# Performance work log

Measured on AMD Instinct MI355X. Metric: run time of the kernel, lower is better.

Reference implementation:

```python
import jax, jax.numpy as jnp
import numpy as np
from jax.scipy import special

B, N, DIM, H, DK, DV, F = 2, 1536, 1536, 8, 64, 64, 192


def _pos_embed(seq_len, feat):
    """Enformer relative positional basis: [2*seq_len-1, feat]."""
    per = feat // 6  # 3 basis families x (symmetric, antisymmetric)
    d = jnp.arange(-seq_len + 1, seq_len, dtype=jnp.float32)
    ad = jnp.abs(d)[:, None]  # [2N-1, 1]
    # exponential decay, log-spaced half lives
    half_life = 2.0 ** jnp.linspace(3.0, float(np.log2(seq_len)), per)
    expo = jnp.exp(-jnp.log(2.0) / half_life * ad)
    # central binary mask
    widths = 2.0 ** jnp.arange(1, per + 1, dtype=jnp.float32) - 1.0
    cmask = (widths > ad).astype(jnp.float32)
    # gamma pdf basis
    stddev = seq_len / (2.0 * per)
    start_mean = seq_len / per
    mean = jnp.linspace(start_mean, float(seq_len), per)
    conc = (mean / stddev) ** 2
    rate = mean / stddev ** 2
    log_unnorm = special.xlogy(conc - 1.0, ad) - rate * ad
    log_norm = special.gammaln(conc) - conc * jnp.log(rate)
    probs = jnp.exp(log_unnorm - log_norm) + 1e-8
    gamma = probs / jnp.max(probs, axis=-1, keepdims=True)
    emb = jnp.concatenate([expo, cmask, gamma], axis=-1)
    emb = jnp.concatenate([emb, jnp.sign(d)[:, None] * emb], axis=-1)
    return emb.astype(jnp.float32)


def _relative_shift(x):
    # x: [B, H, N, 2N-1] -> [B, H, N, N] (Transformer-XL shift)
    b, h, t1, t2 = x.shape
    x = jnp.pad(x, ((0, 0), (0, 0), (0, 0), (1, 0)))  # [B,H,N,2N]
    x = x.reshape(b, h, t2 + 1, t1)[:, :, 1:, :].reshape(b, h, t1, t2)
    return x[..., : (t2 + 2) // 2]


def setup_inputs() -> dict:
    key = jax.random.key(0)
    ks = jax.random.split(key, 8)
    s = 0.02
    return {
        "x": jax.random.normal(ks[0], (B, N, DIM), dtype=jnp.float32),
        "Wq": jax.random.normal(ks[1], (DIM, H * DK), dtype=jnp.float32) * s,
        "Wk": jax.random.normal(ks[2], (DIM, H * DK), dtype=jnp.float32) * s,
        "Wv": jax.random.normal(ks[3], (DIM, H * DV), dtype=jnp.float32) * s,
        "Wrel": jax.random.normal(ks[4], (F, H * DK), dtype=jnp.float32) * s,
        "Wout": jax.random.normal(ks[5], (H * DV, DIM), dtype=jnp.float32) * s,
        "bout": jnp.zeros((DIM,), dtype=jnp.float32),
        "rel_content_bias": jax.random.normal(ks[6], (1, H, 1, DK), dtype=jnp.float32),
        "rel_pos_bias": jax.random.normal(ks[7], (1, H, 1, DK), dtype=jnp.float32),
        "pos_embed": _pos_embed(N, F),  # [2N-1, F] buffer
    }


def reference(x, Wq, Wk, Wv, Wrel, Wout, bout, rel_content_bias, rel_pos_bias, pos_embed):
    b, n, _ = x.shape
    h, dk = rel_content_bias.shape[1], rel_content_bias.shape[3]
    dv = Wv.shape[1] // h
    scale = dk ** -0.5
    q = (x @ Wq).reshape(b, n, h, dk).transpose(0, 2, 1, 3) * scale  # [b,h,n,dk]
    k = (x @ Wk).reshape(b, n, h, dk).transpose(0, 2, 1, 3)
    v = (x @ Wv).reshape(b, n, h, dv).transpose(0, 2, 1, 3)
    content_logits = jnp.einsum('bhid,bhjd->bhij', q + rel_content_bias, k)
    rel_k = (pos_embed @ Wrel).reshape(-1, h, dk).transpose(1, 0, 2)  # [h,2n-1,dk]
    rel_logits = jnp.einsum('bhid,hjd->bhij', q + rel_pos_bias, rel_k)  # [b,h,n,2n-1]
    rel_logits = _relative_shift(rel_logits)  # [b,h,n,n]
    attn = jax.nn.softmax(content_logits + rel_logits, axis=-1)
    out = jnp.einsum('bhij,bhjd->bhid', attn, v)
    out = out.transpose(0, 2, 1, 3).reshape(b, n, h * dv)
    return out @ Wout + bout
```

## Files before the change

### kernel.cpp

```cpp
#include <hip/hip_runtime.h>

#define NSEQ  1536
#define HEADS 8
#define NREL  3071
#define NRELP 3072

typedef __bf16 bf16;
typedef __bf16 bf16x8 __attribute__((ext_vector_type(8)));
typedef __bf16 bf16x4 __attribute__((ext_vector_type(4)));
typedef float  f32x4  __attribute__((ext_vector_type(4)));

static __device__ __forceinline__ f32x4 mfma16(bf16x8 a, bf16x8 b, f32x4 c) {
  return __builtin_amdgcn_mfma_f32_16x16x32_bf16(a, b, c, 0, 0, 0);
}

static __device__ __forceinline__ void gload_lds16(const bf16* g, bf16* l) {
  __builtin_amdgcn_global_load_lds((const __attribute__((address_space(1))) void*)g,
                                   (__attribute__((address_space(3))) void*)l, 16, 0, 0);
}

#define DPP_F(v, ctrl) __int_as_float(__builtin_amdgcn_update_dpp(0, __float_as_int(v), ctrl, 0xF, 0xF, true))
static __device__ __forceinline__ float rowsum16(float v) {
  v += DPP_F(v, 0xB1);
  v += DPP_F(v, 0x4E);
  v += DPP_F(v, 0x124);
  v += DPP_F(v, 0x128);
  return v;
}

__global__ __launch_bounds__(256) void prep(const float* __restrict__ x, const float* __restrict__ pos,
                                            const float* __restrict__ Wq, const float* __restrict__ Wk,
                                            const float* __restrict__ Wv, const float* __restrict__ Wout,
                                            const float* __restrict__ Wrel,
                                            bf16* __restrict__ xb, bf16* __restrict__ posb,
                                            bf16* __restrict__ WT, bf16* __restrict__ WoT,
                                            bf16* __restrict__ WrT) {
  int blk = blockIdx.x;
  if (blk < 4608) {
    int i = blk * 256 + threadIdx.x;
    float4 v = ((const float4*)x)[i];
    bf16x4 o;
    o[0] = (bf16)v.x; o[1] = (bf16)v.y; o[2] = (bf16)v.z; o[3] = (bf16)v.w;
    ((bf16x4*)xb)[i] = o;
    return;
  }
  blk -= 4608;
  if (blk < 576) {
    int i = blk * 256 + threadIdx.x;
    if (i < (NREL * 192 / 4)) {
      float4 v = ((const float4*)pos)[i];
      bf16x4 o;
      o[0] = (bf16)v.x; o[1] = (bf16)v.y; o[2] = (bf16)v.z; o[3] = (bf16)v.w;
      ((bf16x4*)posb)[i] = o;
    }
    return;
  }
  blk -= 576;
  const float* in; bf16* out; int C, ostride, orowoff, cx, ry;
  if (blk < 768)       { in = Wq;   out = WT;  C = 512;  ostride = 1536; orowoff = 0;    cx = blk % 16; ry = blk / 16; }
  else if (blk < 1536) { blk -= 768;  in = Wk;   out = WT;  C = 512;  ostride = 1536; orowoff = 512;  cx = blk % 16; ry = blk / 16; }
  else if (blk < 2304) { blk -= 1536; in = Wv;   out = WT;  C = 512;  ostride = 1536; orowoff = 1024; cx = blk % 16; ry = blk / 16; }
  else if (blk < 3072) { blk -= 2304; in = Wout; out = WoT; C = 1536; ostride = 512;  orowoff = 0;    cx = blk % 48; ry = blk / 48; }
  else                 { blk -= 3072; in = Wrel; out = WrT; C = 512;  ostride = 192;  orowoff = 0;    cx = blk % 16; ry = blk / 16; }
  __shared__ float t[32][33];
  int tx = threadIdx.x & 31, ty = threadIdx.x >> 5;
  int r0 = ry * 32, c0 = cx * 32;
#pragma unroll
  for (int i = 0; i < 4; i++)
    t[ty + 8 * i][tx] = in[(size_t)(r0 + ty + 8 * i) * C + c0 + tx];
  __syncthreads();
#pragma unroll
  for (int i = 0; i < 4; i++)
    out[(size_t)(c0 + ty + 8 * i + orowoff) * ostride + r0 + tx] = (bf16)t[tx][ty + 8 * i];
}

static __device__ __forceinline__ void gemm_core(const bf16* __restrict__ A, const bf16* __restrict__ BT,
                                                 int Klen, int ldk, int m0, int n0, int M,
                                                 bf16* sa, bf16* sb, f32x4 acc[4][2]) {
  int tid = threadIdx.x, wave = tid >> 6, lane = tid & 63;
  int l15 = lane & 15, quad = lane >> 4;
  int lrow = lane >> 3, lcg = lane & 7;
  for (int k0 = 0; k0 < Klen; k0 += 64) {
    __syncthreads();
#pragma unroll
    for (int t = 0; t < 2; t++) {
      int row = wave * 16 + t * 8 + lrow;
      int ra = m0 + row; if (ra > M - 1) ra = M - 1;
      gload_lds16(A + (size_t)ra * ldk + k0 + ((lcg ^ (row & 7)) * 8), sa + (wave * 16 + t * 8) * 64);
    }
#pragma unroll
    for (int t = 0; t < 4; t++) {
      int row = wave * 32 + t * 8 + lrow;
      gload_lds16(BT + (size_t)(n0 + row) * ldk + k0 + ((lcg ^ (row & 7)) * 8), sb + (wave * 32 + t * 8) * 64);
    }
    __syncthreads();
#pragma unroll
    for (int kq = 0; kq < 2; kq++) {
      bf16x8 af[4], bfr[2];
#pragma unroll
      for (int rt = 0; rt < 4; rt++) {
        int row = rt * 16 + l15;
        af[rt] = *(const bf16x8*)&sa[row * 64 + (((kq * 4 + quad) ^ (row & 7)) * 8)];
      }
#pragma unroll
      for (int ct = 0; ct < 2; ct++) {
        int row = wave * 32 + ct * 16 + l15;
        bfr[ct] = *(const bf16x8*)&sb[row * 64 + (((kq * 4 + quad) ^ (row & 7)) * 8)];
      }
#pragma unroll
      for (int ct = 0; ct < 2; ct++)
#pragma unroll
        for (int rt = 0; rt < 4; rt++)
          acc[rt][ct] = mfma16(af[rt], bfr[ct], acc[rt][ct]);
    }
  }
}

__global__ __launch_bounds__(256) void gemm_qkv(const bf16* __restrict__ xb, const bf16* __restrict__ WT,
                                                const float* __restrict__ cb, const float* __restrict__ pb,
                                                bf16* __restrict__ qc, bf16* __restrict__ qp,
                                                bf16* __restrict__ kb, bf16* __restrict__ vt) {
  __shared__ __align__(16) bf16 sa[64 * 64];
  __shared__ __align__(16) bf16 sb[128 * 64];
  __shared__ __align__(16) bf16 tv[64 * 130];
  int tid = threadIdx.x, wave = tid >> 6, lane = tid & 63;
  int l15 = lane & 15, quad = lane >> 4;
  int m0 = blockIdx.x * 64, n0 = blockIdx.y * 128;
  f32x4 acc[4][2] = {};
  gemm_core(xb, WT, 1536, 1536, m0, n0, 3072, sa, sb, acc);
  int b = m0 / NSEQ, nseq0 = m0 % NSEQ;
  if (blockIdx.y < 8) {
    bool isq = blockIdx.y < 4;
#pragma unroll
    for (int rt = 0; rt < 4; rt++)
#pragma unroll
      for (int ct = 0; ct < 2; ct++)
#pragma unroll
        for (int r = 0; r < 4; r++) {
          int row = nseq0 + rt * 16 + quad * 4 + r;
          int colg = n0 + wave * 32 + ct * 16 + l15;
          int col = colg & 511;
          int h = col >> 6, d = col & 63;
          size_t o = ((size_t)(b * 8 + h) * NSEQ + row) * 64 + d;
          float v = acc[rt][ct][r];
          if (isq) {
            float qv = v * 0.125f;
            qc[o] = (bf16)(qv + cb[col]);
            qp[o] = (bf16)(qv + pb[col]);
          } else {
            kb[o] = (bf16)v;
          }
        }
  } else {
#pragma unroll
    for (int rt = 0; rt < 4; rt++)
#pragma unroll
      for (int ct = 0; ct < 2; ct++)
#pragma unroll
        for (int r = 0; r < 4; r++)
          tv[(rt * 16 + quad * 4 + r) * 130 + wave * 32 + ct * 16 + l15] = (bf16)acc[rt][ct][r];
    __syncthreads();
    int n = tid & 63, c0v = tid >> 6;
    int hbase = (blockIdx.y - 8) * 2;
#pragma unroll
    for (int hh = 0; hh < 2; hh++)
#pragma unroll
      for (int i = 0; i < 16; i++) {
        int dv = i * 4 + c0v;
        vt[((size_t)(b * 8 + hbase + hh) * 64 + dv) * NSEQ + nseq0 + n] = tv[n * 130 + hh * 64 + dv];
      }
  }
}

__global__ __launch_bounds__(256) void gemm_rel(const bf16* __restrict__ posb, const bf16* __restrict__ WrT,
                                                bf16* __restrict__ rk) {
  __shared__ __align__(16) bf16 sa[64 * 64];
  __shared__ __align__(16) bf16 sb[128 * 64];
  int tid = threadIdx.x, wave = tid >> 6, lane = tid & 63;
  int l15 = lane & 15, quad = lane >> 4;
  int m0 = blockIdx.x * 64, n0 = blockIdx.y * 128;
  f32x4 acc[4][2] = {};
  gemm_core(posb, WrT, 192, 192, m0, n0, NREL, sa, sb, acc);
#pragma unroll
  for (int rt = 0; rt < 4; rt++)
#pragma unroll
    for (int ct = 0; ct < 2; ct++)
#pragma unroll
      for (int r = 0; r < 4; r++) {
        int row = m0 + rt * 16 + quad * 4 + r;
        if (row < NREL) {
          int col = n0 + wave * 32 + ct * 16 + l15;
          rk[((size_t)(col >> 6) * NRELP + row) * 64 + (col & 63)] = (bf16)acc[rt][ct][r];
        }
      }
}

__global__ __launch_bounds__(256) void gemm_out(const bf16* __restrict__ A, const bf16* __restrict__ BT,
                                                float* __restrict__ C, const float* __restrict__ bias) {
  __shared__ __align__(16) bf16 sa[64 * 64];
  __shared__ __align__(16) bf16 sb[128 * 64];
  int tid = threadIdx.x, wave = tid >> 6, lane = tid & 63;
  int l15 = lane & 15, quad = lane >> 4;
  int m0 = blockIdx.x * 64, n0 = blockIdx.y * 128;
  f32x4 acc[4][2] = {};
  gemm_core(A, BT, 512, 512, m0, n0, 3072, sa, sb, acc);
#pragma unroll
  for (int rt = 0; rt < 4; rt++)
#pragma unroll
    for (int ct = 0; ct < 2; ct++)
#pragma unroll
      for (int r = 0; r < 4; r++) {
        int row = m0 + rt * 16 + quad * 4 + r;
        int col = n0 + wave * 32 + ct * 16 + l15;
        C[(size_t)row * 1536 + col] = acc[rt][ct][r] + bias[col];
      }
}

__global__ __launch_bounds__(256, 4) void attn(const bf16* __restrict__ qc, const bf16* __restrict__ qp,
                                               const bf16* __restrict__ kb, const bf16* __restrict__ vt,
                                               const bf16* __restrict__ rk,
                                               float* __restrict__ Opart, float* __restrict__ mlp) {
  __shared__ __align__(16) bf16 sk[64 * 64];
  __shared__ __align__(16) bf16 sv[64 * 64];
  __shared__ __align__(16) bf16 srel[128 * 64];
  __shared__ __align__(16) bf16 pls[4][16 * 72];
  int qb = blockIdx.x, bh = blockIdx.y, kz = blockIdx.z;
  int h = bh & 7;
  int i0 = qb * 64;
  int wave = threadIdx.x >> 6, lane = threadIdx.x & 63;
  int l15 = lane & 15, quad = lane >> 4;
  int lrow = lane >> 3, lcg = lane & 7;
  const bf16* qcb = qc + (size_t)bh * NSEQ * 64;
  const bf16* qpb = qp + (size_t)bh * NSEQ * 64;
  const bf16* kbb = kb + (size_t)bh * NSEQ * 64;
  const bf16* vtb = vt + (size_t)bh * 64 * NSEQ;
  const bf16* rkh = rk + (size_t)h * NRELP * 64;
  bf16* plsw = pls[wave];

  int qrow = i0 + wave * 16 + l15;
  bf16x8 aqc0 = *(const bf16x8*)(qcb + (size_t)qrow * 64 + quad * 8);
  bf16x8 aqc1 = *(const bf16x8*)(qcb + (size_t)qrow * 64 + 32 + quad * 8);
  bf16x8 aqp0 = *(const bf16x8*)(qpb + (size_t)qrow * 64 + quad * 8);
  bf16x8 aqp1 = *(const bf16x8*)(qpb + (size_t)qrow * 64 + 32 + quad * 8);

  int bidx[4];
  bool hisel[4];
#pragma unroll
  for (int r = 0; r < 4; r++) {
    int rl = quad * 4 + r;
    bidx[r] = (quad * 16 + ((l15 + 15 - rl) & 15)) << 2;
    hisel[r] = l15 > rl;
  }

  f32x4 acco[4] = {};
  float li[4] = {0.0f, 0.0f, 0.0f, 0.0f};

  int locbase = (3 - wave) * 16;
  for (int jt = 0; jt < 12; jt++) {
    int j0 = kz * 768 + jt * 64;
    int Rbase = 1472 + j0 - i0;
    __syncthreads();
#pragma unroll
    for (int t = 0; t < 2; t++) {
      int row = wave * 16 + t * 8 + lrow;
      gload_lds16(kbb + (size_t)(j0 + row) * 64 + ((lcg ^ (row & 7)) * 8),
                  sk + (wave * 16 + t * 8) * 64);
    }
#pragma unroll
    for (int t = 0; t < 2; t++) {
      int row = wave * 16 + t * 8 + lrow;
      gload_lds16(vtb + (size_t)row * NSEQ + j0 + ((lcg ^ (row & 7)) * 8),
                  sv + (wave * 16 + t * 8) * 64);
    }
#pragma unroll
    for (int t = 0; t < 4; t++) {
      int loc = wave * 32 + t * 8 + lrow;
      gload_lds16(rkh + (size_t)(Rbase + loc) * 64 + ((lcg ^ (loc & 7)) * 8),
                  srel + (wave * 32 + t * 8) * 64);
    }
    __syncthreads();
    f32x4 s[4] = {};
#pragma unroll
    for (int c = 0; c < 4; c++) {
      int key = c * 16 + l15;
      bf16x8 b0 = *(const bf16x8*)&sk[key * 64 + ((quad ^ (key & 7)) * 8)];
      bf16x8 b1 = *(const bf16x8*)&sk[key * 64 + (((4 + quad) ^ (key & 7)) * 8)];
      s[c] = mfma16(aqc0, b0, s[c]);
      s[c] = mfma16(aqc1, b1, s[c]);
    }
    f32x4 sb5[5];
#pragma unroll
    for (int cc = 0; cc < 5; cc++) {
      int loc = locbase + cc * 16 + l15;
      bf16x8 b0 = *(const bf16x8*)&srel[loc * 64 + ((quad ^ (loc & 7)) * 8)];
      bf16x8 b1 = *(const bf16x8*)&srel[loc * 64 + (((4 + quad) ^ (loc & 7)) * 8)];
      f32x4 z = {};
      z = mfma16(aqp0, b0, z);
      sb5[cc] = mfma16(aqp1, b1, z);
    }
#pragma unroll
    for (int r = 0; r < 4; r++) {
      float bp[5];
#pragma unroll
      for (int cc = 0; cc < 5; cc++)
        bp[cc] = __int_as_float(__builtin_amdgcn_ds_bpermute(bidx[r], __float_as_int(sb5[cc][r])));
#pragma unroll
      for (int c = 0; c < 4; c++)
        s[c][r] += hisel[r] ? bp[c + 1] : bp[c];
    }
#pragma unroll
    for (int c = 0; c < 4; c++)
#pragma unroll
      for (int r = 0; r < 4; r++) {
        float p = __expf(s[c][r] - 8.0f);
        bf16 pbh = (bf16)p;
        li[r] += (float)pbh;
        plsw[(quad * 4 + r) * 72 + c * 16 + l15] = pbh;
      }
#pragma unroll
    for (int ks = 0; ks < 2; ks++) {
      bf16x8 ap = *(const bf16x8*)&plsw[l15 * 72 + ks * 32 + quad * 8];
#pragma unroll
      for (int c = 0; c < 4; c++) {
        int dv = c * 16 + l15;
        bf16x8 bv = *(const bf16x8*)&sv[dv * 64 + (((ks * 4 + quad) ^ (dv & 7)) * 8)];
        acco[c] = mfma16(ap, bv, acco[c]);
      }
    }
  }
#pragma unroll
  for (int r = 0; r < 4; r++)
    li[r] = rowsum16(li[r]);
  int qt16 = qb * 4 + wave;
  size_t pbase = ((size_t)(bh * 96 + qt16) * 2 + kz);
#pragma unroll
  for (int c = 0; c < 4; c++)
#pragma unroll
    for (int r = 0; r < 4; r++)
      Opart[pbase * 1024 + (quad * 4 + r) * 64 + c * 16 + l15] = acco[c][r];
  if (l15 == 0) {
#pragma unroll
    for (int r = 0; r < 4; r++)
      mlp[pbase * 16 + quad * 4 + r] = li[r];
  }
}

__global__ void attn_merge(const float* __restrict__ Opart, const float* __restrict__ mlp,
                           bf16* __restrict__ O) {
  int qt = blockIdx.x, bh = blockIdx.y;
  int b = bh >> 3, h = bh & 7;
  int col = threadIdx.x & 63, rg = threadIdx.x >> 6;
  size_t base = (size_t)(bh * 96 + qt) * 2;
#pragma unroll
  for (int rr = 0; rr < 4; rr++) {
    int row = rg * 4 + rr;
    float L = mlp[base * 16 + row] + mlp[(base + 1) * 16 + row];
    float v = Opart[base * 1024 + row * 64 + col] + Opart[(base + 1) * 1024 + row * 64 + col];
    O[((size_t)(b * NSEQ + qt * 16 + row) * 8 + h) * 64 + col] = (bf16)(v / L);
  }
}

extern "C" void kernel_launch(void* const* d_in, const int* in_sizes, int n_in,
                              void* d_out, int out_size, void* d_ws, size_t ws_size,
                              hipStream_t stream) {
  const float* x    = (const float*)d_in[0];
  const float* Wq   = (const float*)d_in[1];
  const float* Wk   = (const float*)d_in[2];
  const float* Wv   = (const float*)d_in[3];
  const float* Wrel = (const float*)d_in[4];
  const float* Wout = (const float*)d_in[5];
  const float* bout = (const float*)d_in[6];
  const float* cb   = (const float*)d_in[7];
  const float* pb   = (const float*)d_in[8];
  const float* pos  = (const float*)d_in[9];
  float* out = (float*)d_out;

  char* ws = (char*)d_ws;
  size_t off = 0;
  auto alloc = [&](size_t bytes) {
    char* p = ws + off;
    off = (off + bytes + 255) & ~(size_t)255;
    return p;
  };
  bf16*  xb    = (bf16*)alloc(3072UL * 1536 * 2);
  bf16*  WT    = (bf16*)alloc(1536UL * 1536 * 2);
  bf16*  WoT   = (bf16*)alloc(1536UL * 512 * 2);
  bf16*  WrT   = (bf16*)alloc(512UL * 192 * 2);
  bf16*  posb  = (bf16*)alloc((size_t)NREL * 192 * 2);
  bf16*  qcb   = (bf16*)alloc(16UL * NSEQ * 64 * 2);
  bf16*  qpb   = (bf16*)alloc(16UL * NSEQ * 64 * 2);
  bf16*  kbb   = (bf16*)alloc(16UL * NSEQ * 64 * 2);
  bf16*  vtb   = (bf16*)alloc(16UL * NSEQ * 64 * 2);
  bf16*  rkb   = (bf16*)alloc(8UL * NRELP * 64 * 2);
  bf16*  Ob    = (bf16*)alloc(3072UL * 512 * 2);
  float* Opart = (float*)alloc(16UL * 96 * 2 * 1024 * 4);
  float* mlpw  = (float*)alloc(16UL * 96 * 2 * 16 * 4);

  prep<<<dim3(8352), 256, 0, stream>>>(x, pos, Wq, Wk, Wv, Wout, Wrel, xb, posb, WT, WoT, WrT);
  gemm_qkv<<<dim3(48, 12), 256, 0, stream>>>(xb, WT, cb, pb, qcb, qpb, kbb, vtb);
  gemm_rel<<<dim3(48, 4), 256, 0, stream>>>(posb, WrT, rkb);
  attn<<<dim3(24, 16, 2), 256, 0, stream>>>(qcb, qpb, kbb, vtb, rkb, Opart, mlpw);
  attn_merge<<<dim3(96, 16), 256, 0, stream>>>(Opart, mlpw, Ob);
  gemm_out<<<dim3(48, 12), 256, 0, stream>>>(Ob, WoT, out, bout);
}
```

Measured before the change: 176.1 us.

## Reuse relative-key window across tiles, fold log2e into q, use exp2

The attention loop now keeps the 128-row relative-key window in a two-slot ring buffer. Each iteration loads only the new 64-row block and reuses the half it overlaps with the previous iteration, with one extra block preloaded before the loop. Global and LDS addresses are hoisted into pointers that are bumped each iteration, and the P staging buffer drops its padding in favour of an XOR swizzle. The softmax scale and biases are premultiplied by log2(e) in the projection epilogue, so the kernel can use the native exp2 instead of __expf. The intent is to cut relative-key traffic, address arithmetic and exp cost. The risk is that the more complex ring-buffer indexing and the changed bf16 rounding of the prescaled q could subtly affect accuracy.

```diff
diff --git a/kernel.cpp b/kernel.cpp
--- a/kernel.cpp
+++ b/kernel.cpp
@@ -144,9 +144,9 @@
           size_t o = ((size_t)(b * 8 + h) * NSEQ + row) * 64 + d;
           float v = acc[rt][ct][r];
           if (isq) {
-            float qv = v * 0.125f;
-            qc[o] = (bf16)(qv + cb[col]);
-            qp[o] = (bf16)(qv + pb[col]);
+            float qv = v * 0.18033688011f;
+            qc[o] = (bf16)(qv + cb[col] * 1.44269504089f);
+            qp[o] = (bf16)(qv + pb[col] * 1.44269504089f);
           } else {
             kb[o] = (bf16)v;
           }
@@ -223,7 +223,7 @@
   __shared__ __align__(16) bf16 sk[64 * 64];
   __shared__ __align__(16) bf16 sv[64 * 64];
   __shared__ __align__(16) bf16 srel[128 * 64];
-  __shared__ __align__(16) bf16 pls[4][16 * 72];
+  __shared__ __align__(16) bf16 pls[4][16 * 64];
   int qb = blockIdx.x, bh = blockIdx.y, kz = blockIdx.z;
   int h = bh & 7;
   int i0 = qb * 64;
@@ -252,51 +252,58 @@
     hisel[r] = l15 > rl;
   }
 
+  int swz = (lcg ^ lrow) * 8;
+  int jb = 23 + kz * 12 - qb;
+  const bf16* pK = kbb + (size_t)(kz * 768 + wave * 16 + lrow) * 64 + swz;
+  const bf16* pV = vtb + (size_t)(wave * 16 + lrow) * NSEQ + kz * 768 + swz;
+  const bf16* pR = rkh + (size_t)(jb + 1) * 4096 + (size_t)(wave * 16 + lrow) * 64 + swz;
+  bf16* dK = sk + wave * 1024;
+  bf16* dV = sv + wave * 1024;
+
+  {
+    const bf16* pP = rkh + (size_t)jb * 4096 + (size_t)(wave * 16 + lrow) * 64 + swz;
+    bf16* dP = srel + ((jb & 1) * 64 + wave * 16) * 64;
+#pragma unroll
+    for (int t = 0; t < 2; t++)
+      gload_lds16(pP + t * 512, dP + t * 512);
+  }
+  int pxor = (jb & 1) << 6;
+
+  int swzA = (quad ^ (l15 & 7)) * 8;
+  int swzB = ((4 + quad) ^ (l15 & 7)) * 8;
+  int rb0 = (3 - wave) * 16 + l15;
+  int pxl = (l15 >> 1) << 3;
+  const bf16* plr = plsw + l15 * 64;
+
   f32x4 acco[4] = {};
   float li[4] = {0.0f, 0.0f, 0.0f, 0.0f};
 
-  int locbase = (3 - wave) * 16;
   for (int jt = 0; jt < 12; jt++) {
-    int j0 = kz * 768 + jt * 64;
-    int Rbase = 1472 + j0 - i0;
     __syncthreads();
 #pragma unroll
-    for (int t = 0; t < 2; t++) {
-      int row = wave * 16 + t * 8 + lrow;
-      gload_lds16(kbb + (size_t)(j0 + row) * 64 + ((lcg ^ (row & 7)) * 8),
-                  sk + (wave * 16 + t * 8) * 64);
-    }
-#pragma unroll
-    for (int t = 0; t < 2; t++) {
-      int row = wave * 16 + t * 8 + lrow;
-      gload_lds16(vtb + (size_t)row * NSEQ + j0 + ((lcg ^ (row & 7)) * 8),
-                  sv + (wave * 16 + t * 8) * 64);
-    }
-#pragma unroll
-    for (int t = 0; t < 4; t++) {
-      int loc = wave * 32 + t * 8 + lrow;
-      gload_lds16(rkh + (size_t)(Rbase + loc) * 64 + ((lcg ^ (loc & 7)) * 8),
-                  srel + (wave * 32 + t * 8) * 64);
+    for (int t = 0; t < 2; t++) gload_lds16(pK + t * 512, dK + t * 512);
+#pragma unroll
+    for (int t = 0; t < 2; t++) gload_lds16(pV + (size_t)t * 8 * NSEQ, dV + t * 512);
+    {
+      bf16* dR = srel + (pxor ^ 64) * 64 + wave * 1024;
+#pragma unroll
+      for (int t = 0; t < 2; t++) gload_lds16(pR + t * 512, dR + t * 512);
     }
     __syncthreads();
     f32x4 s[4] = {};
 #pragma unroll
     for (int c = 0; c < 4; c++) {
-      int key = c * 16 + l15;
-      bf16x8 b0 = *(const bf16x8*)&sk[key * 64 + ((quad ^ (key & 7)) * 8)];
-      bf16x8 b1 = *(const bf16x8*)&sk[key * 64 + (((4 + quad) ^ (key & 7)) * 8)];
-      s[c] = mfma16(aqc0, b0, s[c]);
-      s[c] = mfma16(aqc1, b1, s[c]);
+      const bf16* kp = sk + (c * 16 + l15) * 64;
+      s[c] = mfma16(aqc0, *(const bf16x8*)(kp + swzA), s[c]);
+      s[c] = mfma16(aqc1, *(const bf16x8*)(kp + swzB), s[c]);
     }
     f32x4 sb5[5];
 #pragma unroll
     for (int cc = 0; cc < 5; cc++) {
-      int loc = locbase + cc * 16 + l15;
-      bf16x8 b0 = *(const bf16x8*)&srel[loc * 64 + ((quad ^ (loc & 7)) * 8)];
-      bf16x8 b1 = *(const bf16x8*)&srel[loc * 64 + (((4 + quad) ^ (loc & 7)) * 8)];
+      const bf16* rp = srel + ((rb0 + cc * 16) ^ pxor) * 64;
       f32x4 z = {};
-      z = mfma16(aqp0, b0, z);
-      sb5[cc] = mfma16(aqp1, b1, z);
+      z = mfma16(aqp0, *(const bf16x8*)(rp + swzA), z);
+      sb5[cc] = mfma16(aqp1, *(const bf16x8*)(rp + swzB), z);
     }
 #pragma unroll
     for (int r = 0; r < 4; r++) {
@@ -312,21 +319,22 @@
     for (int c = 0; c < 4; c++)
 #pragma unroll
       for (int r = 0; r < 4; r++) {
-        float p = __expf(s[c][r] - 8.0f);
+        float p = __builtin_amdgcn_exp2f(s[c][r] - 11.5415603f);
         bf16 pbh = (bf16)p;
         li[r] += (float)pbh;
-        plsw[(quad * 4 + r) * 72 + c * 16 + l15] = pbh;
+        int prow = quad * 4 + r;
+        plsw[prow * 64 + ((c * 16 + l15) ^ ((prow >> 1) << 3))] = pbh;
       }
 #pragma unroll
     for (int ks = 0; ks < 2; ks++) {
-      bf16x8 ap = *(const bf16x8*)&plsw[l15 * 72 + ks * 32 + quad * 8];
+      bf16x8 ap = *(const bf16x8*)(plr + ((ks * 32 + quad * 8) ^ pxl));
 #pragma unroll
       for (int c = 0; c < 4; c++) {
-        int dv = c * 16 + l15;
-        bf16x8 bv = *(const bf16x8*)&sv[dv * 64 + (((ks * 4 + quad) ^ (dv & 7)) * 8)];
-        acco[c] = mfma16(ap, bv, acco[c]);
-      }
-    }
+        const bf16* vp = sv + (c * 16 + l15) * 64;
+        acco[c] = mfma16(ap, *(const bf16x8*)(vp + (ks ? swzB : swzA)), acco[c]);
+      }
+    }
+    pK += 4096; pV += 64; pR += 4096; pxor ^= 64;
   }
 #pragma unroll
   for (int r = 0; r < 4; r++)
```

New measurement: 175.1 us. No clear change (-0.6%).
